# Kernel optimization log

Measured on AMD Instinct MI355X. Metric: run time of the kernel, lower is better.

## Reference

```python
import jax, jax.numpy as jnp
import numpy as np

# Blade metric for Cl(1,3) inner product <~A B>_0: sign per basis blade =
# (-1)^{k(k-1)/2} * prod(eta_ii) with eta = diag(1,-1,-1,-1).
# Order: 1 | e0 e1 e2 e3 | e01 e02 e03 e12 e13 e23 | e012 e013 e023 e123 | e0123
BLADE_METRIC = jnp.array(
    [1.0,
     1.0, -1.0, -1.0, -1.0,
     1.0, 1.0, 1.0, -1.0, -1.0, -1.0,
     -1.0, -1.0, -1.0, 1.0,
     -1.0],
    dtype=jnp.float32,
)

B, H, N, MVC, SC = 8, 8, 1024, 8, 32


def setup_inputs() -> dict:
    key = jax.random.key(0)
    ks = jax.random.split(key, 6)
    mv_shape = (B, H, N, MVC, 16)
    s_shape = (B, H, N, SC)
    return {
        "q_mv": jax.random.normal(ks[0], mv_shape, dtype=jnp.float32),
        "k_mv": jax.random.normal(ks[1], mv_shape, dtype=jnp.float32),
        "v_mv": jax.random.normal(ks[2], mv_shape, dtype=jnp.float32),
        "q_s": jax.random.normal(ks[3], s_shape, dtype=jnp.float32),
        "k_s": jax.random.normal(ks[4], s_shape, dtype=jnp.float32),
        "v_s": jax.random.normal(ks[5], s_shape, dtype=jnp.float32),
    }


def reference(q_mv, k_mv, v_mv, q_s, k_s, v_s):
    *lead, n_out, mvc, _ = q_mv.shape
    n_in = k_mv.shape[-3]
    sc = q_s.shape[-1]
    d = 16 * mvc + sc  # total feature dim used for the softmax scale

    # Apply GA blade metric to queries, flatten mv channels, concat scalars.
    qf = jnp.concatenate(
        [(q_mv * BLADE_METRIC).reshape(*lead, n_out, mvc * 16), q_s], axis=-1
    )
    kf = jnp.concatenate([k_mv.reshape(*lead, n_in, mvc * 16), k_s], axis=-1)
    vf = jnp.concatenate([v_mv.reshape(*lead, n_in, mvc * 16), v_s], axis=-1)

    scores = jnp.einsum("bhid,bhjd->bhij", qf, kf) / jnp.sqrt(
        jnp.asarray(d, dtype=qf.dtype)
    )
    attn = jax.nn.softmax(scores, axis=-1)
    out = jnp.einsum("bhij,bhjd->bhid", attn, vf)

    out_mv = out[..., : mvc * 16].reshape(*lead, n_out, mvc, 16)
    out_s = out[..., mvc * 16 :]
    return out_mv, out_s
```

## Files before the change

### kernel.cpp

```cpp
#include <hip/hip_runtime.h>

typedef __attribute__((ext_vector_type(8))) _Float16 f16x8;
typedef __attribute__((ext_vector_type(4))) float f32x4;

#define BHn 64
#define Nn 1024

static constexpr int kOutMvElems = 8 * 8 * 1024 * 128;
static constexpr float kScaleLog2e = 0.11405506f;
static constexpr unsigned kNegMask = 0xBF1Cu;
static constexpr int kBlob = 20480;

typedef __attribute__((address_space(1))) const void* gas1_t;
typedef __attribute__((address_space(3))) void* las3_t;
__device__ __forceinline__ void dma16(const _Float16* g, _Float16* l) {
  __builtin_amdgcn_global_load_lds((gas1_t)g, (las3_t)l, 16, 0, 0);
}

__global__ __launch_bounds__(256) void pack_kernel(const float* __restrict__ kmv,
                                                   const float* __restrict__ ks,
                                                   const float* __restrict__ vmv,
                                                   const float* __restrict__ vs,
                                                   _Float16* __restrict__ KV) {
  __shared__ _Float16 tk[64][184];
  __shared__ _Float16 tv[160][72];
  const int kt = blockIdx.x;
  const int bh = blockIdx.y;
  const int tid = threadIdx.x;
#pragma unroll
  for (int i = 0; i < 5; ++i) {
    int s = tid + 256 * i;
    int key = s / 20, p = s - key * 20;
    int row = bh * Nn + kt * 64 + key;
    const float* src = (p < 16) ? (kmv + (size_t)row * 128 + p * 8)
                                : (ks + (size_t)row * 32 + (p - 16) * 8);
    float4 a = *(const float4*)src;
    float4 b = *(const float4*)(src + 4);
    f16x8 h;
    h[0] = (_Float16)a.x; h[1] = (_Float16)a.y; h[2] = (_Float16)a.z; h[3] = (_Float16)a.w;
    h[4] = (_Float16)b.x; h[5] = (_Float16)b.y; h[6] = (_Float16)b.z; h[7] = (_Float16)b.w;
    *(f16x8*)&tk[key][p * 8] = h;
  }
  for (int s = tid; s < 64 * 40; s += 256) {
    int key = s / 40, p = s - key * 40;
    int row = bh * Nn + kt * 64 + key;
    const float* src = (p < 32) ? (vmv + (size_t)row * 128 + p * 4)
                                : (vs + (size_t)row * 32 + (p - 32) * 4);
    float4 v = *(const float4*)src;
    int d = p * 4;
    tv[d + 0][key] = (_Float16)v.x;
    tv[d + 1][key] = (_Float16)v.y;
    tv[d + 2][key] = (_Float16)v.z;
    tv[d + 3][key] = (_Float16)v.w;
  }
  __syncthreads();
  _Float16* dst = KV + ((size_t)bh * 16 + kt) * kBlob;
#pragma unroll
  for (int i = 0; i < 5; ++i) {
    int u = tid + 256 * i;
    int p = u >> 6, key = u & 63;
    f16x8 h = *(const f16x8*)&tk[key][p * 8];
    *(f16x8*)&dst[p * 512 + key * 8] = h;
  }
#pragma unroll
  for (int i = 0; i < 5; ++i) {
    int u = tid + 256 * i;
    int s = u / 160, d = u - s * 160;
    int c32 = (s >> 2) * 32, gg = s & 3;
    f16x8 h;
#pragma unroll
    for (int i2 = 0; i2 < 8; ++i2) {
      int key = c32 + ((i2 < 4) ? (gg * 4 + i2) : (16 + gg * 4 + (i2 - 4)));
      h[i2] = tv[d][key];
    }
    *(f16x8*)&dst[10240 + u * 8] = h;
  }
}

__global__ __launch_bounds__(256, 2) void geo_attn_kernel(const float* __restrict__ qmv,
                                                          const float* __restrict__ qs,
                                                          const _Float16* __restrict__ KV,
                                                          float* __restrict__ out) {
  __shared__ __align__(16) _Float16 kv[2 * kBlob];

  const int b = blockIdx.x;
  const int sw = (b & 7) * 64 + (b >> 3);
  const int qb = sw & 7;
  const int bh = sw >> 3;

  const int tid = threadIdx.x;
  const int w = tid >> 6;
  const int l = tid & 63;
  const int g = l >> 4;
  const int nn = l & 15;

  const _Float16* blob0 = KV + (size_t)bh * 16 * kBlob;

  int kbase[5];
#pragma unroll
  for (int c = 0; c < 5; ++c) kbase[c] = (4 * c + g) * 512 + nn * 8;
  int vbase[2];
#pragma unroll
  for (int ch = 0; ch < 2; ++ch) vbase[ch] = 10240 + (4 * ch + g) * 1280 + nn * 8;

  f16x8 qf[2][5];
#pragma unroll
  for (int q2 = 0; q2 < 2; ++q2) {
    const size_t qbase = (size_t)(bh * Nn + qb * 128 + w * 32 + q2 * 16 + nn);
#pragma unroll
    for (int c = 0; c < 5; ++c) {
      const float* src = (c < 4) ? (qmv + qbase * 128 + c * 32 + 8 * g)
                                 : (qs + qbase * 32 + 8 * g);
      float4 a = *(const float4*)src;
      float4 bb = *(const float4*)(src + 4);
      float x[8] = {a.x, a.y, a.z, a.w, bb.x, bb.y, bb.z, bb.w};
#pragma unroll
      for (int i = 0; i < 8; ++i) {
        float v = x[i] * kScaleLog2e;
        if (c < 4) {
          int idx = ((g & 1) << 3) + i;
          v = ((kNegMask >> idx) & 1u) ? -v : v;
        }
        qf[q2][c][i] = (_Float16)v;
      }
    }
  }

  f32x4 acc[2][10];
#pragma unroll
  for (int q2 = 0; q2 < 2; ++q2)
#pragma unroll
    for (int j = 0; j < 10; ++j) acc[q2][j] = (f32x4){0.f, 0.f, 0.f, 0.f};
  float Ma = 12.f, Mb = 12.f, La = 0.f, Lb = 0.f;

  f32x4 sa[4], sb[4];
  f16x8 paf[2], pbf[2];

  const int laneOff = l * 8 + w * 512;
  auto stage = [&](int t, int buf) {
    const _Float16* src = blob0 + (size_t)t * kBlob + laneOff;
    _Float16* dst = &kv[buf * kBlob + w * 512];
#pragma unroll
    for (int i = 0; i < 10; ++i) dma16(src + i * 2048, dst + i * 2048);
  };
  auto do_qk = [&](int buf) {
    const _Float16* kb_ = &kv[buf * kBlob];
#pragma unroll
    for (int kb = 0; kb < 4; ++kb) {
      sa[kb] = (f32x4){0.f, 0.f, 0.f, 0.f};
      sb[kb] = (f32x4){0.f, 0.f, 0.f, 0.f};
    }
#pragma unroll
    for (int c = 0; c < 5; ++c) {
      f16x8 kf[4];
#pragma unroll
      for (int kb = 0; kb < 4; ++kb) kf[kb] = *(const f16x8*)&kb_[kbase[c] + kb * 128];
#pragma unroll
      for (int kb = 0; kb < 4; ++kb) {
        sa[kb] = __builtin_amdgcn_mfma_f32_16x16x32_f16(kf[kb], qf[0][c], sa[kb], 0, 0, 0);
        sb[kb] = __builtin_amdgcn_mfma_f32_16x16x32_f16(kf[kb], qf[1][c], sb[kb], 0, 0, 0);
      }
    }
  };
  auto do_pv = [&](int buf) {
    const _Float16* vb_ = &kv[buf * kBlob];
#pragma unroll
    for (int ch = 0; ch < 2; ++ch)
#pragma unroll
      for (int j = 0; j < 10; ++j) {
        f16x8 vb = *(const f16x8*)&vb_[vbase[ch] + j * 128];
        acc[0][j] = __builtin_amdgcn_mfma_f32_16x16x32_f16(paf[ch], vb, acc[0][j], 0, 0, 0);
        acc[1][j] = __builtin_amdgcn_mfma_f32_16x16x32_f16(pbf[ch], vb, acc[1][j], 0, 0, 0);
      }
  };
  auto do_softmax = [&]() {
    float lma = fmaxf(fmaxf(fmaxf(fmaxf(sa[0][0], sa[0][1]), fmaxf(sa[0][2], sa[0][3])),
                            fmaxf(fmaxf(sa[1][0], sa[1][1]), fmaxf(sa[1][2], sa[1][3]))),
                      fmaxf(fmaxf(fmaxf(sa[2][0], sa[2][1]), fmaxf(sa[2][2], sa[2][3])),
                            fmaxf(fmaxf(sa[3][0], sa[3][1]), fmaxf(sa[3][2], sa[3][3]))));
    float lmb = fmaxf(fmaxf(fmaxf(fmaxf(sb[0][0], sb[0][1]), fmaxf(sb[0][2], sb[0][3])),
                            fmaxf(fmaxf(sb[1][0], sb[1][1]), fmaxf(sb[1][2], sb[1][3]))),
                      fmaxf(fmaxf(fmaxf(sb[2][0], sb[2][1]), fmaxf(sb[2][2], sb[2][3])),
                            fmaxf(fmaxf(sb[3][0], sb[3][1]), fmaxf(sb[3][2], sb[3][3]))));
    bool need = (lma - Ma > 8.f) || (lmb - Mb > 8.f);
    if (__any((int)need)) {
      float pma = fmaxf(lma, __shfl_xor(lma, 16));
      pma = fmaxf(pma, __shfl_xor(pma, 32));
      float pmb = fmaxf(lmb, __shfl_xor(lmb, 16));
      pmb = fmaxf(pmb, __shfl_xor(pmb, 32));
      float nMa = fmaxf(Ma, pma); float fsa = exp2f(Ma - nMa); Ma = nMa;
      float nMb = fmaxf(Mb, pmb); float fsb = exp2f(Mb - nMb); Mb = nMb;
      La *= fsa; Lb *= fsb;
      float fa[4], fb[4];
#pragma unroll
      for (int r = 0; r < 4; ++r) {
        fa[r] = __shfl(fsa, 4 * g + r, 16);
        fb[r] = __shfl(fsb, 4 * g + r, 16);
      }
#pragma unroll
      for (int j = 0; j < 10; ++j)
#pragma unroll
        for (int r = 0; r < 4; ++r) {
          acc[0][j][r] *= fa[r];
          acc[1][j][r] *= fb[r];
        }
    }
    float rsa = 0.f, rsb = 0.f;
#pragma unroll
    for (int kb = 0; kb < 4; ++kb) {
      const int ch = kb >> 1, off = (kb & 1) * 4;
#pragma unroll
      for (int r = 0; r < 4; ++r) {
        float pa_ = exp2f(sa[kb][r] - Ma);
        float pb_ = exp2f(sb[kb][r] - Mb);
        rsa += pa_; rsb += pb_;
        paf[ch][off + r] = (_Float16)pa_;
        pbf[ch][off + r] = (_Float16)pb_;
      }
    }
    La += rsa;
    Lb += rsb;
  };

  stage(0, 0);
  __syncthreads();

  for (int t = 0; t < 16; ++t) {
    const int cur = t & 1;
    if (t < 15) stage(t + 1, cur ^ 1);
    __builtin_amdgcn_s_setprio(1);
    do_qk(cur);
    __builtin_amdgcn_s_setprio(0);
    do_softmax();
    __builtin_amdgcn_s_setprio(1);
    do_pv(cur);
    __builtin_amdgcn_s_setprio(0);
    __syncthreads();
  }

  La += __shfl_xor(La, 16); La += __shfl_xor(La, 32);
  Lb += __shfl_xor(Lb, 16); Lb += __shfl_xor(Lb, 32);
  float ria = 1.f / La, rib = 1.f / Lb;
  float ra[4], rb_[4];
#pragma unroll
  for (int r = 0; r < 4; ++r) {
    ra[r] = __shfl(ria, 4 * g + r, 16);
    rb_[r] = __shfl(rib, 4 * g + r, 16);
  }
  const int row0 = bh * Nn + qb * 128 + w * 32;
#pragma unroll
  for (int j = 0; j < 10; ++j) {
    const int d = 16 * j + nn;
#pragma unroll
    for (int r = 0; r < 4; ++r) {
      float v0 = acc[0][j][r] * ra[r];
      float v1 = acc[1][j][r] * rb_[r];
      const int r0 = row0 + 4 * g + r;
      const int r1 = row0 + 16 + 4 * g + r;
      if (d < 128) {
        out[(size_t)r0 * 128 + d] = v0;
        out[(size_t)r1 * 128 + d] = v1;
      } else {
        out[(size_t)kOutMvElems + (size_t)r0 * 32 + (d - 128)] = v0;
        out[(size_t)kOutMvElems + (size_t)r1 * 32 + (d - 128)] = v1;
      }
    }
  }
}

extern "C" void kernel_launch(void* const* d_in, const int* in_sizes, int n_in,
                              void* d_out, int out_size, void* d_ws, size_t ws_size,
                              hipStream_t stream) {
  const float* qmv = (const float*)d_in[0];
  const float* kmv = (const float*)d_in[1];
  const float* vmv = (const float*)d_in[2];
  const float* qs = (const float*)d_in[3];
  const float* ks = (const float*)d_in[4];
  const float* vs = (const float*)d_in[5];
  float* out = (float*)d_out;

  _Float16* KV = (_Float16*)d_ws;

  pack_kernel<<<dim3(16, BHn), dim3(256), 0, stream>>>(kmv, ks, vmv, vs, KV);
  geo_attn_kernel<<<dim3(512), dim3(256), 0, stream>>>(qmv, qs, KV, out);
}
```

Baseline: 85.56 us.

## Use 8 waves per block with 16 queries each and lazy softmax rescale

```diff
diff --git a/kernel.cpp b/kernel.cpp
--- a/kernel.cpp
+++ b/kernel.cpp
@@ -77,7 +77,7 @@
   }
 }
 
-__global__ __launch_bounds__(256, 2) void geo_attn_kernel(const float* __restrict__ qmv,
+__global__ __launch_bounds__(512, 2) void geo_attn_kernel(const float* __restrict__ qmv,
                                                           const float* __restrict__ qs,
                                                           const _Float16* __restrict__ KV,
                                                           float* __restrict__ out) {
@@ -103,10 +103,9 @@
 #pragma unroll
   for (int ch = 0; ch < 2; ++ch) vbase[ch] = 10240 + (4 * ch + g) * 1280 + nn * 8;
 
-  f16x8 qf[2][5];
-#pragma unroll
-  for (int q2 = 0; q2 < 2; ++q2) {
-    const size_t qbase = (size_t)(bh * Nn + qb * 128 + w * 32 + q2 * 16 + nn);
+  f16x8 qf[5];
+  {
+    const size_t qbase = (size_t)(bh * Nn + qb * 128 + w * 16 + nn);
 #pragma unroll
     for (int c = 0; c < 5; ++c) {
       const float* src = (c < 4) ? (qmv + qbase * 128 + c * 32 + 8 * g)
@@ -121,45 +120,38 @@
           int idx = ((g & 1) << 3) + i;
           v = ((kNegMask >> idx) & 1u) ? -v : v;
         }
-        qf[q2][c][i] = (_Float16)v;
-      }
-    }
-  }
-
-  f32x4 acc[2][10];
-#pragma unroll
-  for (int q2 = 0; q2 < 2; ++q2)
-#pragma unroll
-    for (int j = 0; j < 10; ++j) acc[q2][j] = (f32x4){0.f, 0.f, 0.f, 0.f};
-  float Ma = 12.f, Mb = 12.f, La = 0.f, Lb = 0.f;
-
-  f32x4 sa[4], sb[4];
-  f16x8 paf[2], pbf[2];
+        qf[c][i] = (_Float16)v;
+      }
+    }
+  }
+
+  f32x4 acc[10];
+#pragma unroll
+  for (int j = 0; j < 10; ++j) acc[j] = (f32x4){0.f, 0.f, 0.f, 0.f};
+  float Ma = 12.f, La = 0.f;
+
+  f32x4 sa[4];
+  f16x8 paf[2];
 
   const int laneOff = l * 8 + w * 512;
   auto stage = [&](int t, int buf) {
     const _Float16* src = blob0 + (size_t)t * kBlob + laneOff;
     _Float16* dst = &kv[buf * kBlob + w * 512];
 #pragma unroll
-    for (int i = 0; i < 10; ++i) dma16(src + i * 2048, dst + i * 2048);
+    for (int i = 0; i < 5; ++i) dma16(src + i * 4096, dst + i * 4096 + (l * 8 - l * 8));
   };
   auto do_qk = [&](int buf) {
     const _Float16* kb_ = &kv[buf * kBlob];
 #pragma unroll
-    for (int kb = 0; kb < 4; ++kb) {
-      sa[kb] = (f32x4){0.f, 0.f, 0.f, 0.f};
-      sb[kb] = (f32x4){0.f, 0.f, 0.f, 0.f};
-    }
+    for (int kb = 0; kb < 4; ++kb) sa[kb] = (f32x4){0.f, 0.f, 0.f, 0.f};
 #pragma unroll
     for (int c = 0; c < 5; ++c) {
       f16x8 kf[4];
 #pragma unroll
       for (int kb = 0; kb < 4; ++kb) kf[kb] = *(const f16x8*)&kb_[kbase[c] + kb * 128];
 #pragma unroll
-      for (int kb = 0; kb < 4; ++kb) {
-        sa[kb] = __builtin_amdgcn_mfma_f32_16x16x32_f16(kf[kb], qf[0][c], sa[kb], 0, 0, 0);
-        sb[kb] = __builtin_amdgcn_mfma_f32_16x16x32_f16(kf[kb], qf[1][c], sb[kb], 0, 0, 0);
-      }
+      for (int kb = 0; kb < 4; ++kb)
+        sa[kb] = __builtin_amdgcn_mfma_f32_16x16x32_f16(kf[kb], qf[c], sa[kb], 0, 0, 0);
     }
   };
   auto do_pv = [&](int buf) {
@@ -169,57 +161,53 @@
 #pragma unroll
       for (int j = 0; j < 10; ++j) {
         f16x8 vb = *(const f16x8*)&vb_[vbase[ch] + j * 128];
-        acc[0][j] = __builtin_amdgcn_mfma_f32_16x16x32_f16(paf[ch], vb, acc[0][j], 0, 0, 0);
-        acc[1][j] = __builtin_amdgcn_mfma_f32_16x16x32_f16(pbf[ch], vb, acc[1][j], 0, 0, 0);
+        acc[j] = __builtin_amdgcn_mfma_f32_16x16x32_f16(paf[ch], vb, acc[j], 0, 0, 0);
       }
   };
   auto do_softmax = [&]() {
-    float lma = fmaxf(fmaxf(fmaxf(fmaxf(sa[0][0], sa[0][1]), fmaxf(sa[0][2], sa[0][3])),
-                            fmaxf(fmaxf(sa[1][0], sa[1][1]), fmaxf(sa[1][2], sa[1][3]))),
-                      fmaxf(fmaxf(fmaxf(sa[2][0], sa[2][1]), fmaxf(sa[2][2], sa[2][3])),
-                            fmaxf(fmaxf(sa[3][0], sa[3][1]), fmaxf(sa[3][2], sa[3][3]))));
-    float lmb = fmaxf(fmaxf(fmaxf(fmaxf(sb[0][0], sb[0][1]), fmaxf(sb[0][2], sb[0][3])),
-                            fmaxf(fmaxf(sb[1][0], sb[1][1]), fmaxf(sb[1][2], sb[1][3]))),
-                      fmaxf(fmaxf(fmaxf(sb[2][0], sb[2][1]), fmaxf(sb[2][2], sb[2][3])),
-                            fmaxf(fmaxf(sb[3][0], sb[3][1]), fmaxf(sb[3][2], sb[3][3]))));
-    bool need = (lma - Ma > 8.f) || (lmb - Mb > 8.f);
-    if (__any((int)need)) {
-      float pma = fmaxf(lma, __shfl_xor(lma, 16));
-      pma = fmaxf(pma, __shfl_xor(pma, 32));
-      float pmb = fmaxf(lmb, __shfl_xor(lmb, 16));
-      pmb = fmaxf(pmb, __shfl_xor(pmb, 32));
-      float nMa = fmaxf(Ma, pma); float fsa = exp2f(Ma - nMa); Ma = nMa;
-      float nMb = fmaxf(Mb, pmb); float fsb = exp2f(Mb - nMb); Mb = nMb;
-      La *= fsa; Lb *= fsb;
-      float fa[4], fb[4];
-#pragma unroll
-      for (int r = 0; r < 4; ++r) {
-        fa[r] = __shfl(fsa, 4 * g + r, 16);
-        fb[r] = __shfl(fsb, 4 * g + r, 16);
-      }
-#pragma unroll
-      for (int j = 0; j < 10; ++j)
-#pragma unroll
-        for (int r = 0; r < 4; ++r) {
-          acc[0][j][r] *= fa[r];
-          acc[1][j][r] *= fb[r];
-        }
-    }
-    float rsa = 0.f, rsb = 0.f;
+    float rsa = 0.f;
 #pragma unroll
     for (int kb = 0; kb < 4; ++kb) {
       const int ch = kb >> 1, off = (kb & 1) * 4;
 #pragma unroll
       for (int r = 0; r < 4; ++r) {
         float pa_ = exp2f(sa[kb][r] - Ma);
-        float pb_ = exp2f(sb[kb][r] - Mb);
-        rsa += pa_; rsb += pb_;
+        rsa += pa_;
         paf[ch][off + r] = (_Float16)pa_;
-        pbf[ch][off + r] = (_Float16)pb_;
+      }
+    }
+    if (__builtin_expect(__any((int)(rsa > 3.2e4f)), 0)) {
+      float lma = sa[0][0];
+#pragma unroll
+      for (int kb = 0; kb < 4; ++kb)
+#pragma unroll
+        for (int r = 0; r < 4; ++r) lma = fmaxf(lma, sa[kb][r]);
+      lma = fmaxf(lma, __shfl_xor(lma, 16));
+      lma = fmaxf(lma, __shfl_xor(lma, 32));
+      float nMa = fmaxf(Ma, lma);
+      float fsa = exp2f(Ma - nMa);
+      Ma = nMa;
+      La *= fsa;
+      float fa[4];
+#pragma unroll
+      for (int r = 0; r < 4; ++r) fa[r] = __shfl(fsa, 4 * g + r, 16);
+#pragma unroll
+      for (int j = 0; j < 10; ++j)
+#pragma unroll
+        for (int r = 0; r < 4; ++r) acc[j][r] *= fa[r];
+      rsa = 0.f;
+#pragma unroll
+      for (int kb = 0; kb < 4; ++kb) {
+        const int ch = kb >> 1, off = (kb & 1) * 4;
+#pragma unroll
+        for (int r = 0; r < 4; ++r) {
+          float pa_ = exp2f(sa[kb][r] - Ma);
+          rsa += pa_;
+          paf[ch][off + r] = (_Float16)pa_;
+        }
       }
     }
     La += rsa;
-    Lb += rsb;
   };
 
   stage(0, 0);
@@ -238,32 +226,24 @@
     __syncthreads();
   }
 
-  La += __shfl_xor(La, 16); La += __shfl_xor(La, 32);
-  Lb += __shfl_xor(Lb, 16); Lb += __shfl_xor(Lb, 32);
-  float ria = 1.f / La, rib = 1.f / Lb;
-  float ra[4], rb_[4];
-#pragma unroll
-  for (int r = 0; r < 4; ++r) {
-    ra[r] = __shfl(ria, 4 * g + r, 16);
-    rb_[r] = __shfl(rib, 4 * g + r, 16);
-  }
-  const int row0 = bh * Nn + qb * 128 + w * 32;
+  La += __shfl_xor(La, 16);
+  La += __shfl_xor(La, 32);
+  float ria = 1.f / La;
+  float ra[4];
+#pragma unroll
+  for (int r = 0; r < 4; ++r) ra[r] = __shfl(ria, 4 * g + r, 16);
+  const int row0 = bh * Nn + qb * 128 + w * 16;
 #pragma unroll
   for (int j = 0; j < 10; ++j) {
     const int d = 16 * j + nn;
 #pragma unroll
     for (int r = 0; r < 4; ++r) {
-      float v0 = acc[0][j][r] * ra[r];
-      float v1 = acc[1][j][r] * rb_[r];
+      float v0 = acc[j][r] * ra[r];
       const int r0 = row0 + 4 * g + r;
-      const int r1 = row0 + 16 + 4 * g + r;
-      if (d < 128) {
+      if (d < 128)
         out[(size_t)r0 * 128 + d] = v0;
-        out[(size_t)r1 * 128 + d] = v1;
-      } else {
+      else
         out[(size_t)kOutMvElems + (size_t)r0 * 32 + (d - 128)] = v0;
-        out[(size_t)kOutMvElems + (size_t)r1 * 32 + (d - 128)] = v1;
-      }
     }
   }
 }
@@ -282,5 +262,5 @@
   _Float16* KV = (_Float16*)d_ws;
 
   pack_kernel<<<dim3(16, BHn), dim3(256), 0, stream>>>(kmv, ks, vmv, vs, KV);
-  geo_attn_kernel<<<dim3(512), dim3(256), 0, stream>>>(qmv, qs, KV, out);
-}
+  geo_attn_kernel<<<dim3(512), dim3(512), 0, stream>>>(qmv, qs, KV, out);
+}
```

Result: slower. 91.41 us (+6.8%).
